# Kernel tuning notes

Measured on AMD Instinct MI355X. Metric: run time of the kernel, lower is better.

## Reference

```python
import jax, jax.numpy as jnp
import numpy as np

DIM = 1024
HEADS = 16
HEAD_DIM = DIM // HEADS
MLP_HID = 4 * DIM
EPS = 1e-5


def layer_norm(x, g, b):
    mu = jnp.mean(x, axis=-1, keepdims=True)
    var = jnp.mean(jnp.square(x - mu), axis=-1, keepdims=True)
    return (x - mu) * jax.lax.rsqrt(var + EPS) * g + b


def setup_inputs() -> dict:
    key = jax.random.key(0)
    ks = jax.random.split(key, 8)
    s_in = 1.0 / np.sqrt(DIM)
    s_hid = 1.0 / np.sqrt(MLP_HID)
    return {
        "x": jax.random.normal(ks[0], (4, 2048, DIM), dtype=jnp.float32),
        "qkv_w": jax.random.uniform(ks[1], (3 * DIM, DIM), jnp.float32, -s_in, s_in),
        "proj_w": jax.random.uniform(ks[2], (DIM, DIM), jnp.float32, -s_in, s_in),
        "proj_b": jnp.zeros((DIM,), jnp.float32),
        "ln1_g": jnp.ones((DIM,), jnp.float32),
        "ln1_b": jnp.zeros((DIM,), jnp.float32),
        "w1": jax.random.uniform(ks[3], (MLP_HID, DIM), jnp.float32, -s_in, s_in),
        "b1": jnp.zeros((MLP_HID,), jnp.float32),
        "prelu_a": jnp.asarray(0.25, jnp.float32),
        "w2": jax.random.uniform(ks[4], (DIM, MLP_HID), jnp.float32, -s_hid, s_hid),
        "b2": jnp.zeros((DIM,), jnp.float32),
        "ln2_g": jnp.ones((DIM,), jnp.float32),
        "ln2_b": jnp.zeros((DIM,), jnp.float32),
    }


def reference(x, qkv_w, proj_w, proj_b, ln1_g, ln1_b, w1, b1, prelu_a, w2, b2, ln2_g, ln2_b):
    B, N, C = x.shape
    scale = HEAD_DIM ** (-0.5)

    # Multi-head self-attention (full NxN scores, softmax over keys)
    qkv = (x @ qkv_w.T).reshape(B, N, 3, HEADS, HEAD_DIM)
    qkv = jnp.transpose(qkv, (2, 0, 3, 1, 4))  # [3, B, H, N, hd]
    q, k, v = qkv[0] * scale, qkv[1], qkv[2]
    attn = jax.nn.softmax(jnp.einsum("bhnd,bhmd->bhnm", q, k), axis=-1)
    o = jnp.einsum("bhnm,bhmd->bhnd", attn, v)
    o = jnp.transpose(o, (0, 2, 1, 3)).reshape(B, N, C)
    o = o @ proj_w.T + proj_b

    # Post-norm residual 1
    x = layer_norm(x + o, ln1_g, ln1_b)

    # MLP: Linear -> (Dropout=identity in eval) -> PReLU -> Linear
    h = x @ w1.T + b1
    h = jnp.where(h >= 0, h, prelu_a * h)
    h = h @ w2.T + b2

    # Post-norm residual 2
    return layer_norm(x + h, ln2_g, ln2_b)
```

## Files before the change

kernel.cpp:

```cpp
#include <hip/hip_runtime.h>


typedef __attribute__((ext_vector_type(8))) short short8;
typedef __attribute__((ext_vector_type(4))) short short4v;
typedef __attribute__((ext_vector_type(4))) float floatx4;
typedef __attribute__((ext_vector_type(4))) int int4v;

__device__ __forceinline__ float bf2f(unsigned short u) {
    return __uint_as_float(((unsigned int)u) << 16);
}
__device__ __forceinline__ unsigned short f2bf(float f) {
    unsigned int u = __float_as_uint(f);
    u += 0x7FFFu + ((u >> 16) & 1u);
    return (unsigned short)(u >> 16);
}
__device__ __forceinline__ int pack2bf(float a, float b) {
    return (int)f2bf(a) | ((int)f2bf(b) << 16);
}
__device__ __forceinline__ unsigned int cvt_pk_bf16(float lo, float hi) {
    unsigned int r;
    asm("v_cvt_pk_bf16_f32 %0, %1, %2" : "=v"(r) : "v"(lo), "v"(hi));
    return r;
}

#define Q_PRESCALE 0.18033688011112043f

#if __has_builtin(__builtin_amdgcn_exp2f)
__device__ __forceinline__ float fast_exp2(float x) { return __builtin_amdgcn_exp2f(x); }
#else
__device__ __forceinline__ float fast_exp2(float x) { return __expf(x * 0.6931471805599453f); }
#endif

#if __has_builtin(__builtin_amdgcn_permlane32_swap) && __has_builtin(__builtin_amdgcn_permlane16_swap)
#define HAVE_PERMLANE 1
#else
#define HAVE_PERMLANE 0
#endif

__device__ __forceinline__ void async16(const unsigned short* g, unsigned short* l) {
    __builtin_amdgcn_global_load_lds(
        (const __attribute__((address_space(1))) unsigned int*)g,
        (__attribute__((address_space(3))) unsigned int*)l, 16, 0, 0);
}

__global__ __launch_bounds__(256)
void cvt_f2b(const float* __restrict__ in, unsigned short* __restrict__ out) {
    const int i = (blockIdx.x * 256 + threadIdx.x) * 4;
    float4 v = *(const float4*)&in[i];
    short4v o;
    o[0] = (short)f2bf(v.x); o[1] = (short)f2bf(v.y);
    o[2] = (short)f2bf(v.z); o[3] = (short)f2bf(v.w);
    *(short4v*)&out[i] = o;
}

__global__ __launch_bounds__(512, 2)
void gemm256(const unsigned short* __restrict__ A,
             const unsigned short* __restrict__ W,
             const float* __restrict__ bias,
             const float* __restrict__ prelu,
             unsigned short* __restrict__ C,
             int N, int K, int qcols, int NNT) {
    __shared__ alignas(16) unsigned short lA[2][256 * 64];
    __shared__ alignas(16) unsigned short lB[2][256 * 64];

    const int nwg = gridDim.x;
    const int orig = blockIdx.x;
    const int q8 = nwg >> 3, r8 = nwg & 7, xx = orig & 7, rest = orig >> 3;
    const int wgid = (xx < r8 ? xx * (q8 + 1) : r8 * (q8 + 1) + (xx - r8) * q8) + rest;
    const int mt = wgid / NNT, nt = wgid % NNT;
    const int m0 = mt * 256, n0 = nt * 256;

    const int tid  = threadIdx.x;
    const int lane = tid & 63;
    const int wave = tid >> 6;
    const int lr = lane & 15, lq = lane >> 4;
    const int wrow = (wave >> 2) * 64;
    const int wcol = (wave & 3) * 32;
    const int srow = lane >> 3;
    const int scol = ((lane & 7) ^ srow) << 3;
    const int kx = lr & 7;

    const int NT = K >> 6;

    floatx4 acc[2][2][4][2] = {};

    auto stA = [&](int d, int tt, int h) {
        #pragma unroll
        for (int it = 0; it < 2; ++it) {
            const int rb = h * 128 + (wave * 2 + it) * 8;
            async16(&A[(size_t)(m0 + rb + srow) * K + tt * 64 + scol], &lA[d][rb * 64]);
        }
    };
    auto stB = [&](int d, int tt, int h) {
        #pragma unroll
        for (int it = 0; it < 2; ++it) {
            const int rb = h * 128 + (wave * 2 + it) * 8;
            async16(&W[(size_t)(n0 + rb + srow) * K + tt * 64 + scol], &lB[d][rb * 64]);
        }
    };

    stA(0, 0, 0); stB(0, 0, 0); stB(0, 0, 1); stA(0, 0, 1);
    stA(1, 1, 0); stB(1, 1, 0); stB(1, 1, 1);
    asm volatile("s_waitcnt vmcnt(6)" ::: "memory");
    __builtin_amdgcn_s_barrier();
    asm volatile("" ::: "memory");

    short8 af[4][2], b0[2][2], b1[2][2];

    for (int t = 0; t < NT; ++t) {
        const int d = t & 1, e = d ^ 1;

        #pragma unroll
        for (int i = 0; i < 4; ++i)
            #pragma unroll
            for (int s = 0; s < 2; ++s)
                af[i][s] = *(const short8*)&lA[d][(wrow + i * 16 + lr) * 64 +
                                                 (((s * 4 + lq) ^ kx) << 3)];
        #pragma unroll
        for (int j = 0; j < 2; ++j)
            #pragma unroll
            for (int s = 0; s < 2; ++s)
                b0[j][s] = *(const short8*)&lB[d][(wcol + j * 16 + lr) * 64 +
                                                 (((s * 4 + lq) ^ kx) << 3)];
        if (t + 1 < NT) stA(e, t + 1, 1);
        __builtin_amdgcn_s_barrier();
        asm volatile("s_waitcnt lgkmcnt(0)" ::: "memory");
        __builtin_amdgcn_s_setprio(1);
        #pragma unroll
        for (int s = 0; s < 2; ++s)
            #pragma unroll
            for (int i = 0; i < 4; ++i)
                #pragma unroll
                for (int j = 0; j < 2; ++j)
                    acc[0][0][i][j] = __builtin_amdgcn_mfma_f32_16x16x32_bf16(
                        af[i][s], b0[j][s], acc[0][0][i][j], 0, 0, 0);
        __builtin_amdgcn_s_setprio(0);
        __builtin_amdgcn_s_barrier();
        asm volatile("" ::: "memory");

        #pragma unroll
        for (int j = 0; j < 2; ++j)
            #pragma unroll
            for (int s = 0; s < 2; ++s)
                b1[j][s] = *(const short8*)&lB[d][(128 + wcol + j * 16 + lr) * 64 +
                                                 (((s * 4 + lq) ^ kx) << 3)];
        if (t + 2 < NT) stA(d, t + 2, 0);
        __builtin_amdgcn_s_barrier();
        asm volatile("s_waitcnt lgkmcnt(0)" ::: "memory");
        __builtin_amdgcn_s_setprio(1);
        #pragma unroll
        for (int s = 0; s < 2; ++s)
            #pragma unroll
            for (int i = 0; i < 4; ++i)
                #pragma unroll
                for (int j = 0; j < 2; ++j)
                    acc[0][1][i][j] = __builtin_amdgcn_mfma_f32_16x16x32_bf16(
                        af[i][s], b1[j][s], acc[0][1][i][j], 0, 0, 0);
        __builtin_amdgcn_s_setprio(0);
        __builtin_amdgcn_s_barrier();
        asm volatile("" ::: "memory");

        #pragma unroll
        for (int i = 0; i < 4; ++i)
            #pragma unroll
            for (int s = 0; s < 2; ++s)
                af[i][s] = *(const short8*)&lA[d][(128 + wrow + i * 16 + lr) * 64 +
                                                 (((s * 4 + lq) ^ kx) << 3)];
        if (t + 2 < NT) stB(d, t + 2, 0);
        __builtin_amdgcn_s_barrier();
        asm volatile("s_waitcnt lgkmcnt(0)" ::: "memory");
        __builtin_amdgcn_s_setprio(1);
        #pragma unroll
        for (int s = 0; s < 2; ++s)
            #pragma unroll
            for (int i = 0; i < 4; ++i)
                #pragma unroll
                for (int j = 0; j < 2; ++j)
                    acc[1][1][i][j] = __builtin_amdgcn_mfma_f32_16x16x32_bf16(
                        af[i][s], b1[j][s], acc[1][1][i][j], 0, 0, 0);
        __builtin_amdgcn_s_setprio(0);
        __builtin_amdgcn_s_barrier();
        asm volatile("" ::: "memory");

        if (t + 2 < NT) stB(d, t + 2, 1);
        __builtin_amdgcn_s_barrier();
        asm volatile("" ::: "memory");
        __builtin_amdgcn_s_setprio(1);
        #pragma unroll
        for (int s = 0; s < 2; ++s)
            #pragma unroll
            for (int i = 0; i < 4; ++i)
                #pragma unroll
                for (int j = 0; j < 2; ++j)
                    acc[1][0][i][j] = __builtin_amdgcn_mfma_f32_16x16x32_bf16(
                        af[i][s], b0[j][s], acc[1][0][i][j], 0, 0, 0);
        __builtin_amdgcn_s_setprio(0);
        if (t + 2 < NT) {
            asm volatile("s_waitcnt vmcnt(6)" ::: "memory");
        } else {
            asm volatile("s_waitcnt vmcnt(0)" ::: "memory");
        }
        __builtin_amdgcn_s_barrier();
        asm volatile("" ::: "memory");
    }

    const bool hasb = (bias != nullptr);
    const bool hasp = (prelu != nullptr);
    const float slope = hasp ? prelu[0] : 0.f;
    #pragma unroll
    for (int mh = 0; mh < 2; ++mh)
        #pragma unroll
        for (int nh = 0; nh < 2; ++nh)
            #pragma unroll
            for (int j = 0; j < 2; ++j) {
                const int gc = n0 + nh * 128 + wcol + j * 16 + lr;
                const float bv = hasb ? bias[gc] : 0.f;
                const float cs = (gc < qcols) ? Q_PRESCALE : 1.f;
                #pragma unroll
                for (int i = 0; i < 4; ++i) {
                    const int gr = m0 + mh * 128 + wrow + i * 16 + lq * 4;
                    #pragma unroll
                    for (int r = 0; r < 4; ++r) {
                        float v = acc[mh][nh][i][j][r] + bv;
                        if (hasp && v < 0.f) v *= slope;
                        C[(size_t)(gr + r) * N + gc] = f2bf(v * cs);
                    }
                }
            }
}

__global__ __launch_bounds__(512, 2)
void gemm128(const unsigned short* __restrict__ A,
             const unsigned short* __restrict__ W,
             const float* __restrict__ bias,
             const float* __restrict__ prelu,
             unsigned short* __restrict__ C,
             int N, int K, int qcols, int NNT) {
    __shared__ alignas(16) unsigned short lA[2][128 * 64];
    __shared__ alignas(16) unsigned short lB[2][256 * 64];

    const int nwg = gridDim.x;
    const int orig = blockIdx.x;
    const int q8 = nwg >> 3, r8 = nwg & 7, xx = orig & 7, rest = orig >> 3;
    const int wgid = (xx < r8 ? xx * (q8 + 1) : r8 * (q8 + 1) + (xx - r8) * q8) + rest;
    const int mt = wgid / NNT, nt = wgid % NNT;
    const int m0 = mt * 128, n0 = nt * 256;

    const int tid  = threadIdx.x;
    const int lane = tid & 63;
    const int wave = tid >> 6;
    const int lr = lane & 15, lq = lane >> 4;
    const int wrow = (wave >> 2) * 64;
    const int wcol = (wave & 3) * 32;
    const int srow = lane >> 3;
    const int scol = ((lane & 7) ^ srow) << 3;
    const int kx = lr & 7;

    const int NT = K >> 6;

    floatx4 acc[2][4][2] = {};

    auto stA = [&](int d, int tt) {
        #pragma unroll
        for (int it = 0; it < 2; ++it) {
            const int rb = (wave * 2 + it) * 8;
            async16(&A[(size_t)(m0 + rb + srow) * K + tt * 64 + scol], &lA[d][rb * 64]);
        }
    };
    auto stB = [&](int d, int tt, int h) {
        #pragma unroll
        for (int it = 0; it < 2; ++it) {
            const int rb = (wave * 2 + it) * 8;
            async16(&W[(size_t)(n0 + h * 128 + rb + srow) * K + tt * 64 + scol],
                    &lB[d][(h * 128 + rb) * 64]);
        }
    };

    stA(0, 0); stB(0, 0, 0); stB(0, 0, 1);
    stA(1, 1); stB(1, 1, 0);
    asm volatile("s_waitcnt vmcnt(4)" ::: "memory");
    __builtin_amdgcn_s_barrier();
    asm volatile("" ::: "memory");

    short8 af[4][2], b0[2][2], b1[2][2];

    for (int t = 0; t < NT; ++t) {
        const int d = t & 1, e = d ^ 1;

        #pragma unroll
        for (int i = 0; i < 4; ++i)
            #pragma unroll
            for (int s = 0; s < 2; ++s)
                af[i][s] = *(const short8*)&lA[d][(wrow + i * 16 + lr) * 64 +
                                                 (((s * 4 + lq) ^ kx) << 3)];
        #pragma unroll
        for (int j = 0; j < 2; ++j)
            #pragma unroll
            for (int s = 0; s < 2; ++s)
                b0[j][s] = *(const short8*)&lB[d][(wcol + j * 16 + lr) * 64 +
                                                 (((s * 4 + lq) ^ kx) << 3)];
        if (t + 1 < NT) stB(e, t + 1, 1);
        __builtin_amdgcn_s_barrier();
        asm volatile("s_waitcnt lgkmcnt(0)" ::: "memory");
        __builtin_amdgcn_s_setprio(1);
        #pragma unroll
        for (int s = 0; s < 2; ++s)
            #pragma unroll
            for (int i = 0; i < 4; ++i)
                #pragma unroll
                for (int j = 0; j < 2; ++j)
                    acc[0][i][j] = __builtin_amdgcn_mfma_f32_16x16x32_bf16(
                        af[i][s], b0[j][s], acc[0][i][j], 0, 0, 0);
        __builtin_amdgcn_s_setprio(0);
        __builtin_amdgcn_s_barrier();
        asm volatile("" ::: "memory");

        #pragma unroll
        for (int j = 0; j < 2; ++j)
            #pragma unroll
            for (int s = 0; s < 2; ++s)
                b1[j][s] = *(const short8*)&lB[d][(128 + wcol + j * 16 + lr) * 64 +
                                                 (((s * 4 + lq) ^ kx) << 3)];
        if (t + 2 < NT) { stA(d, t + 2); stB(d, t + 2, 0); }
        __builtin_amdgcn_s_barrier();
        asm volatile("s_waitcnt lgkmcnt(0)" ::: "memory");
        __builtin_amdgcn_s_setprio(1);
        #pragma unroll
        for (int s = 0; s < 2; ++s)
            #pragma unroll
            for (int i = 0; i < 4; ++i)
                #pragma unroll
                for (int j = 0; j < 2; ++j)
                    acc[1][i][j] = __builtin_amdgcn_mfma_f32_16x16x32_bf16(
                        af[i][s], b1[j][s], acc[1][i][j], 0, 0, 0);
        __builtin_amdgcn_s_setprio(0);
        if (t + 2 < NT) {
            asm volatile("s_waitcnt vmcnt(4)" ::: "memory");
        } else {
            asm volatile("s_waitcnt vmcnt(0)" ::: "memory");
        }
        __builtin_amdgcn_s_barrier();
        asm volatile("" ::: "memory");
    }

    const bool hasb = (bias != nullptr);
    const bool hasp = (prelu != nullptr);
    const float slope = hasp ? prelu[0] : 0.f;
    #pragma unroll
    for (int nh = 0; nh < 2; ++nh)
        #pragma unroll
        for (int j = 0; j < 2; ++j) {
            const int gc = n0 + nh * 128 + wcol + j * 16 + lr;
            const float bv = hasb ? bias[gc] : 0.f;
            const float cs = (gc < qcols) ? Q_PRESCALE : 1.f;
            #pragma unroll
            for (int i = 0; i < 4; ++i) {
                const int gr = m0 + wrow + i * 16 + lq * 4;
                #pragma unroll
                for (int r = 0; r < 4; ++r) {
                    float v = acc[nh][i][j][r] + bv;
                    if (hasp && v < 0.f) v *= slope;
                    C[(size_t)(gr + r) * N + gc] = f2bf(v * cs);
                }
            }
        }
}

__global__ __launch_bounds__(256)
void transpose_v(const unsigned short* __restrict__ qkv,
                 unsigned short* __restrict__ vt) {
    const int kt = blockIdx.x;
    const int bh = blockIdx.y;
    const int b = bh >> 4, h = bh & 15;
    __shared__ unsigned short tile[64 * 65];
    for (int t = threadIdx.x; t < 512; t += 256) {
        const int key = t >> 3, c8 = (t & 7) << 3;
        short8 v8 = *(const short8*)&qkv[((size_t)(b * 2048 + kt * 64 + key)) * 3072 +
                                         2048 + h * 64 + c8];
        #pragma unroll
        for (int e = 0; e < 8; ++e)
            tile[key * 65 + c8 + e] = (unsigned short)v8[e];
    }
    __syncthreads();
    for (int t = threadIdx.x; t < 512; t += 256) {
        const int d = t >> 3, k8 = (t & 7) << 3;
        short8 o;
        #pragma unroll
        for (int e = 0; e < 8; ++e)
            o[e] = (short)tile[(k8 + e) * 65 + d];
        *(short8*)&vt[((size_t)bh * 64 + d) * 2048 + kt * 64 + k8] = o;
    }
}

__global__ __launch_bounds__(256, 2)
void attn_kernel(const unsigned short* __restrict__ qkv,
                 const unsigned short* __restrict__ vt,
                 unsigned short* __restrict__ o_attn) {
    const int id = blockIdx.x;
    const int qg = id >> 6;
    const int bh = id & 63;
    const int b = bh >> 4, h = bh & 15;
    const int tid  = threadIdx.x;
    const int lane = tid & 63;
    const int wave = tid >> 6;
    const int lr = lane & 15;
    const int lq = lane >> 4;
    const int q0 = (qg * 4 + wave) * 64;
    const size_t row0 = (size_t)(b * 2048) * 3072;

    __shared__ alignas(16) unsigned short lK[2][64 * 64];
    __shared__ alignas(16) unsigned short lV[2][64 * 64];

    short8 qf[4][2];
    #pragma unroll
    for (int j = 0; j < 4; ++j)
        #pragma unroll
        for (int s = 0; s < 2; ++s)
            qf[j][s] = *(const short8*)&qkv[row0 + (size_t)(q0 + j * 16 + lr) * 3072 +
                                            h * 64 + s * 32 + lq * 8];

    floatx4 oacc[4][4] = {};
    float l_i[4] = {0.f, 0.f, 0.f, 0.f};

    const int srow = lane >> 3;
    const int scol = (((lane & 7) ^ srow)) << 3;
    const int kx = lr & 7;

    auto stage = [&](int bi, int kc) {
        #pragma unroll
        for (int it2 = 0; it2 < 2; ++it2) {
            const int it = wave * 2 + it2;
            const int row = it * 8 + srow;
            async16(&qkv[row0 + (size_t)(kc + row) * 3072 + 1024 + h * 64 + scol],
                    &lK[bi][it * 512 + lane * 8]);
            async16(&vt[((size_t)bh * 64 + row) * 2048 + kc + scol],
                    &lV[bi][it * 512 + lane * 8]);
        }
    };

    asm volatile("s_waitcnt vmcnt(0)" ::: "memory");
    stage(0, 0);

    #pragma unroll 1
    for (int c = 0; c < 32; ++c) {
        const int cur = c & 1;
        if (c + 1 < 32) {
            stage(cur ^ 1, (c + 1) * 64);
            asm volatile("s_waitcnt vmcnt(4)" ::: "memory");
        } else {
            asm volatile("s_waitcnt vmcnt(0)" ::: "memory");
        }
        __builtin_amdgcn_s_barrier();
        asm volatile("" ::: "memory");

        floatx4 sacc[4][4] = {};
        #pragma unroll
        for (int s = 0; s < 2; ++s) {
            short8 kf[4];
            #pragma unroll
            for (int i = 0; i < 4; ++i) {
                const int r = i * 16 + lr;
                kf[i] = *(const short8*)&lK[cur][r * 64 + (((s * 4 + lq) ^ kx) << 3)];
            }
            #pragma unroll
            for (int i = 0; i < 4; ++i)
                #pragma unroll
                for (int j = 0; j < 4; ++j)
                    sacc[i][j] = __builtin_amdgcn_mfma_f32_16x16x32_bf16(
                        kf[i], qf[j][s], sacc[i][j], 0, 0, 0);
        }

        unsigned int pkd[4][4][2];
        #pragma unroll
        for (int i = 0; i < 4; ++i)
            #pragma unroll
            for (int j = 0; j < 4; ++j) {
                const float e0 = fast_exp2(sacc[i][j][0]);
                const float e1 = fast_exp2(sacc[i][j][1]);
                const float e2 = fast_exp2(sacc[i][j][2]);
                const float e3 = fast_exp2(sacc[i][j][3]);
                l_i[j] += (e0 + e1) + (e2 + e3);
                pkd[i][j][0] = cvt_pk_bf16(e0, e1);
                pkd[i][j][1] = cvt_pk_bf16(e2, e3);
            }

        #pragma unroll
        for (int s = 0; s < 2; ++s) {
            short8 vf[4];
            #pragma unroll
            for (int i = 0; i < 4; ++i) {
                const int r = i * 16 + lr;
                vf[i] = *(const short8*)&lV[cur][r * 64 + (((s * 4 + lq) ^ kx) << 3)];
            }
            short8 bq[4];
            #pragma unroll
            for (int j = 0; j < 4; ++j) {
                int4v iv;
#if HAVE_PERMLANE
                auto p0 = __builtin_amdgcn_permlane32_swap(
                    pkd[2 * s][j][0], pkd[2 * s + 1][j][0], false, false);
                auto w0 = __builtin_amdgcn_permlane16_swap(p0[0], p0[1], false, false);
                auto p1 = __builtin_amdgcn_permlane32_swap(
                    pkd[2 * s][j][1], pkd[2 * s + 1][j][1], false, false);
                auto w1 = __builtin_amdgcn_permlane16_swap(p1[0], p1[1], false, false);
                iv[0] = (int)w0[0]; iv[1] = (int)w1[0];
                iv[2] = (int)w0[1]; iv[3] = (int)w1[1];
#else
                const int src0 = lr + ((lq & 1) * 2) * 16;
                const int src1 = src0 + 16;
                const bool hi = (lq >> 1) != 0;
                int a0 = __shfl((int)pkd[2 * s][j][0], src0, 64);
                int c0 = __shfl((int)pkd[2 * s + 1][j][0], src0, 64);
                int a1 = __shfl((int)pkd[2 * s][j][1], src0, 64);
                int c1 = __shfl((int)pkd[2 * s + 1][j][1], src0, 64);
                int a2 = __shfl((int)pkd[2 * s][j][0], src1, 64);
                int c2 = __shfl((int)pkd[2 * s + 1][j][0], src1, 64);
                int a3 = __shfl((int)pkd[2 * s][j][1], src1, 64);
                int c3 = __shfl((int)pkd[2 * s + 1][j][1], src1, 64);
                iv[0] = hi ? c0 : a0;
                iv[1] = hi ? c1 : a1;
                iv[2] = hi ? c2 : a2;
                iv[3] = hi ? c3 : a3;
#endif
                bq[j] = __builtin_bit_cast(short8, iv);
            }
            #pragma unroll
            for (int j = 0; j < 4; ++j)
                #pragma unroll
                for (int i = 0; i < 4; ++i)
                    oacc[i][j] = __builtin_amdgcn_mfma_f32_16x16x32_bf16(
                        vf[i], bq[j], oacc[i][j], 0, 0, 0);
        }

        asm volatile("s_waitcnt lgkmcnt(0)" ::: "memory");
        __builtin_amdgcn_s_barrier();
        asm volatile("" ::: "memory");
    }

    #pragma unroll
    for (int j = 0; j < 4; ++j) {
        l_i[j] += __shfl_xor(l_i[j], 16, 64);
        l_i[j] += __shfl_xor(l_i[j], 32, 64);
        const float rl = 1.f / l_i[j];
        const int q = q0 + j * 16 + lr;
        #pragma unroll
        for (int i = 0; i < 4; ++i) {
            int2 pk;
            pk.x = pack2bf(oacc[i][j][0] * rl, oacc[i][j][1] * rl);
            pk.y = pack2bf(oacc[i][j][2] * rl, oacc[i][j][3] * rl);
            *(int2*)&o_attn[((size_t)(b * 2048 + q)) * 1024 + h * 64 + i * 16 + lq * 4] = pk;
        }
    }
}

__global__ __launch_bounds__(256)
void ln_f32_bf16(const float* __restrict__ x,
                 const unsigned short* __restrict__ res,
                 const float* __restrict__ g,
                 const float* __restrict__ bta,
                 unsigned short* __restrict__ out) {
    const int row = blockIdx.x;
    const int t = threadIdx.x;
    const size_t base = (size_t)row * 1024;

    float4 xv = *(const float4*)&x[base + t * 4];
    short4v rv = *(const short4v*)&res[base + t * 4];
    float v[4] = { xv.x + bf2f((unsigned short)rv[0]),
                   xv.y + bf2f((unsigned short)rv[1]),
                   xv.z + bf2f((unsigned short)rv[2]),
                   xv.w + bf2f((unsigned short)rv[3]) };
    float s = 0.f, s2 = 0.f;
    #pragma unroll
    for (int k = 0; k < 4; ++k) { s += v[k]; s2 += v[k] * v[k]; }
    #pragma unroll
    for (int off = 32; off > 0; off >>= 1) {
        s  += __shfl_xor(s, off, 64);
        s2 += __shfl_xor(s2, off, 64);
    }
    __shared__ float red[8];
    const int wave = t >> 6;
    if ((t & 63) == 0) { red[wave] = s; red[4 + wave] = s2; }
    __syncthreads();
    s  = red[0] + red[1] + red[2] + red[3];
    s2 = red[4] + red[5] + red[6] + red[7];
    const float mean = s * (1.f / 1024.f);
    const float var  = fmaxf(s2 * (1.f / 1024.f) - mean * mean, 0.f);
    const float inv  = rsqrtf(var + 1e-5f);

    short4v ov;
    #pragma unroll
    for (int k = 0; k < 4; ++k) {
        int c = t * 4 + k;
        ov[k] = (short)f2bf((v[k] - mean) * inv * g[c] + bta[c]);
    }
    *(short4v*)&out[base + t * 4] = ov;
}

__global__ __launch_bounds__(256)
void ln_bf16_f32(const unsigned short* __restrict__ x,
                 const unsigned short* __restrict__ res,
                 const float* __restrict__ g,
                 const float* __restrict__ bta,
                 float* __restrict__ out) {
    const int row = blockIdx.x;
    const int t = threadIdx.x;
    const size_t base = (size_t)row * 1024;

    short4v xv = *(const short4v*)&x[base + t * 4];
    short4v rv = *(const short4v*)&res[base + t * 4];
    float v[4];
    float s = 0.f, s2 = 0.f;
    #pragma unroll
    for (int k = 0; k < 4; ++k) {
        v[k] = bf2f((unsigned short)xv[k]) + bf2f((unsigned short)rv[k]);
        s += v[k];
        s2 += v[k] * v[k];
    }
    #pragma unroll
    for (int off = 32; off > 0; off >>= 1) {
        s  += __shfl_xor(s, off, 64);
        s2 += __shfl_xor(s2, off, 64);
    }
    __shared__ float red[8];
    const int wave = t >> 6;
    if ((t & 63) == 0) { red[wave] = s; red[4 + wave] = s2; }
    __syncthreads();
    s  = red[0] + red[1] + red[2] + red[3];
    s2 = red[4] + red[5] + red[6] + red[7];
    const float mean = s * (1.f / 1024.f);
    const float var  = fmaxf(s2 * (1.f / 1024.f) - mean * mean, 0.f);
    const float inv  = rsqrtf(var + 1e-5f);

    float4 ov;
    ov.x = (v[0] - mean) * inv * g[t * 4 + 0] + bta[t * 4 + 0];
    ov.y = (v[1] - mean) * inv * g[t * 4 + 1] + bta[t * 4 + 1];
    ov.z = (v[2] - mean) * inv * g[t * 4 + 2] + bta[t * 4 + 2];
    ov.w = (v[3] - mean) * inv * g[t * 4 + 3] + bta[t * 4 + 3];
    *(float4*)&out[base + t * 4] = ov;
}

extern "C" void kernel_launch(void* const* d_in, const int* in_sizes, int n_in,
                              void* d_out, int out_size, void* d_ws, size_t ws_size,
                              hipStream_t stream) {
    const float* x      = (const float*)d_in[0];
    const float* qkv_w  = (const float*)d_in[1];
    const float* proj_w = (const float*)d_in[2];
    const float* proj_b = (const float*)d_in[3];
    const float* ln1_g  = (const float*)d_in[4];
    const float* ln1_b  = (const float*)d_in[5];
    const float* w1     = (const float*)d_in[6];
    const float* b1     = (const float*)d_in[7];
    const float* prelu  = (const float*)d_in[8];
    const float* w2     = (const float*)d_in[9];
    const float* b2     = (const float*)d_in[10];
    const float* ln2_g  = (const float*)d_in[11];
    const float* ln2_b  = (const float*)d_in[12];
    float* out = (float*)d_out;

    char* ws = (char*)d_ws;
    const size_t MB = 1024 * 1024;
    unsigned short* wqkvb  = (unsigned short*)(ws);
    unsigned short* wprojb = (unsigned short*)(ws + 6 * MB);
    unsigned short* w1b    = (unsigned short*)(ws + 8 * MB);
    unsigned short* w2b    = (unsigned short*)(ws + 16 * MB);
    unsigned short* xb     = (unsigned short*)(ws + 24 * MB);
    unsigned short* vtb    = (unsigned short*)(ws + 24 * MB);
    unsigned short* qkvb   = (unsigned short*)(ws + 40 * MB);
    unsigned short* oat    = (unsigned short*)(ws + 88 * MB);
    unsigned short* pout   = (unsigned short*)(ws + 24 * MB);
    unsigned short* x1b    = (unsigned short*)(ws + 40 * MB);
    unsigned short* h1     = (unsigned short*)(ws + 56 * MB);
    unsigned short* h2     = (unsigned short*)(ws + 24 * MB);

    cvt_f2b<<<8192, 256, 0, stream>>>(x,      xb);
    cvt_f2b<<<3072, 256, 0, stream>>>(qkv_w,  wqkvb);
    cvt_f2b<<<1024, 256, 0, stream>>>(proj_w, wprojb);
    cvt_f2b<<<4096, 256, 0, stream>>>(w1,     w1b);
    cvt_f2b<<<4096, 256, 0, stream>>>(w2,     w2b);

    gemm128<<<dim3(64 * 12), 512, 0, stream>>>(xb, wqkvb, nullptr, nullptr,
                                               qkvb, 3072, 1024, 1024, 12);
    transpose_v<<<dim3(32, 64), 256, 0, stream>>>(qkvb, vtb);
    attn_kernel<<<512, 256, 0, stream>>>(qkvb, vtb, oat);
    gemm128<<<dim3(64 * 4), 512, 0, stream>>>(oat, wprojb, proj_b, nullptr,
                                              pout, 1024, 1024, 0, 4);
    ln_f32_bf16<<<8192, 256, 0, stream>>>(x, pout, ln1_g, ln1_b, x1b);
    gemm256<<<dim3(32 * 16), 512, 0, stream>>>(x1b, w1b, b1, prelu,
                                               h1, 4096, 1024, 0, 16);
    gemm128<<<dim3(64 * 4), 512, 0, stream>>>(h1, w2b, b2, nullptr,
                                              h2, 1024, 4096, 0, 4);
    ln_bf16_f32<<<8192, 256, 0, stream>>>(x1b, h2, ln2_g, ln2_b, out);
}
```

Measured before the change: 485.8 us.

## Prefetch next-tile LDS fragments during MFMA phases in both GEMM kernels

Restructures the main loops of the 256- and 128-wide GEMM kernels so that LDS fragment reads for the next phase or next K-tile are issued before or after the preceding MFMA block rather than right before their own use. The explicit lgkmcnt(0) waits are removed, and the vmcnt waits move earlier so that the next tile's A/B fragments can be read at the end of the current iteration. The aim is to hide LDS read latency behind matrix-core work. The risk is subtle ordering hazards between the async global-to-LDS writes and the early reads, which now depend on compiler-inserted waits and the adjusted vmcnt counts.

```diff
diff --git a/kernel.cpp b/kernel.cpp
--- a/kernel.cpp
+++ b/kernel.cpp
@@ -42,6 +42,9 @@
         (const __attribute__((address_space(1))) unsigned int*)g,
         (__attribute__((address_space(3))) unsigned int*)l, 16, 0, 0);
 }
+
+#define BARRIER() do { __builtin_amdgcn_s_barrier(); asm volatile("" ::: "memory"); } while (0)
+#define VMCNT(n)  asm volatile("s_waitcnt vmcnt(" #n ")" ::: "memory")
 
 __global__ __launch_bounds__(256)
 void cvt_f2b(const float* __restrict__ in, unsigned short* __restrict__ out) {
@@ -83,6 +86,7 @@
     const int NT = K >> 6;
 
     floatx4 acc[2][2][4][2] = {};
+    short8 af[4][2], b0[2][2], b1[2][2];
 
     auto stA = [&](int d, int tt, int h) {
         #pragma unroll
@@ -99,110 +103,79 @@
         }
     };
 
+#define RD_AF(dd, half)                                                        \
+    _Pragma("unroll") for (int i = 0; i < 4; ++i)                              \
+    _Pragma("unroll") for (int s = 0; s < 2; ++s)                              \
+        af[i][s] = *(const short8*)&lA[dd][((half) * 128 + wrow + i * 16 + lr) * 64 + \
+                                           (((s * 4 + lq) ^ kx) << 3)]
+#define RD_B0(dd)                                                              \
+    _Pragma("unroll") for (int j = 0; j < 2; ++j)                              \
+    _Pragma("unroll") for (int s = 0; s < 2; ++s)                              \
+        b0[j][s] = *(const short8*)&lB[dd][(wcol + j * 16 + lr) * 64 +         \
+                                           (((s * 4 + lq) ^ kx) << 3)]
+#define RD_B1(dd)                                                              \
+    _Pragma("unroll") for (int j = 0; j < 2; ++j)                              \
+    _Pragma("unroll") for (int s = 0; s < 2; ++s)                              \
+        b1[j][s] = *(const short8*)&lB[dd][(128 + wcol + j * 16 + lr) * 64 +   \
+                                           (((s * 4 + lq) ^ kx) << 3)]
+#define MM256(mh, nh, BB)                                                      \
+    _Pragma("unroll") for (int s = 0; s < 2; ++s)                              \
+    _Pragma("unroll") for (int i = 0; i < 4; ++i)                              \
+    _Pragma("unroll") for (int j = 0; j < 2; ++j)                              \
+        acc[mh][nh][i][j] = __builtin_amdgcn_mfma_f32_16x16x32_bf16(           \
+            af[i][s], BB[j][s], acc[mh][nh][i][j], 0, 0, 0)
+
     stA(0, 0, 0); stB(0, 0, 0); stB(0, 0, 1); stA(0, 0, 1);
     stA(1, 1, 0); stB(1, 1, 0); stB(1, 1, 1);
-    asm volatile("s_waitcnt vmcnt(6)" ::: "memory");
-    __builtin_amdgcn_s_barrier();
-    asm volatile("" ::: "memory");
-
-    short8 af[4][2], b0[2][2], b1[2][2];
+    VMCNT(6);
+    BARRIER();
+    RD_AF(0, 0);
+    RD_B0(0);
 
     for (int t = 0; t < NT; ++t) {
         const int d = t & 1, e = d ^ 1;
 
-        #pragma unroll
-        for (int i = 0; i < 4; ++i)
-            #pragma unroll
-            for (int s = 0; s < 2; ++s)
-                af[i][s] = *(const short8*)&lA[d][(wrow + i * 16 + lr) * 64 +
-                                                 (((s * 4 + lq) ^ kx) << 3)];
-        #pragma unroll
-        for (int j = 0; j < 2; ++j)
-            #pragma unroll
-            for (int s = 0; s < 2; ++s)
-                b0[j][s] = *(const short8*)&lB[d][(wcol + j * 16 + lr) * 64 +
-                                                 (((s * 4 + lq) ^ kx) << 3)];
+        RD_B1(d);
         if (t + 1 < NT) stA(e, t + 1, 1);
-        __builtin_amdgcn_s_barrier();
-        asm volatile("s_waitcnt lgkmcnt(0)" ::: "memory");
+        BARRIER();
         __builtin_amdgcn_s_setprio(1);
-        #pragma unroll
-        for (int s = 0; s < 2; ++s)
-            #pragma unroll
-            for (int i = 0; i < 4; ++i)
-                #pragma unroll
-                for (int j = 0; j < 2; ++j)
-                    acc[0][0][i][j] = __builtin_amdgcn_mfma_f32_16x16x32_bf16(
-                        af[i][s], b0[j][s], acc[0][0][i][j], 0, 0, 0);
+        MM256(0, 0, b0);
         __builtin_amdgcn_s_setprio(0);
-        __builtin_amdgcn_s_barrier();
-        asm volatile("" ::: "memory");
-
-        #pragma unroll
-        for (int j = 0; j < 2; ++j)
-            #pragma unroll
-            for (int s = 0; s < 2; ++s)
-                b1[j][s] = *(const short8*)&lB[d][(128 + wcol + j * 16 + lr) * 64 +
-                                                 (((s * 4 + lq) ^ kx) << 3)];
+        BARRIER();
+
         if (t + 2 < NT) stA(d, t + 2, 0);
-        __builtin_amdgcn_s_barrier();
-        asm volatile("s_waitcnt lgkmcnt(0)" ::: "memory");
+        BARRIER();
         __builtin_amdgcn_s_setprio(1);
-        #pragma unroll
-        for (int s = 0; s < 2; ++s)
-            #pragma unroll
-            for (int i = 0; i < 4; ++i)
-                #pragma unroll
-                for (int j = 0; j < 2; ++j)
-                    acc[0][1][i][j] = __builtin_amdgcn_mfma_f32_16x16x32_bf16(
-                        af[i][s], b1[j][s], acc[0][1][i][j], 0, 0, 0);
+        MM256(0, 1, b1);
         __builtin_amdgcn_s_setprio(0);
-        __builtin_amdgcn_s_barrier();
-        asm volatile("" ::: "memory");
-
-        #pragma unroll
-        for (int i = 0; i < 4; ++i)
-            #pragma unroll
-            for (int s = 0; s < 2; ++s)
-                af[i][s] = *(const short8*)&lA[d][(128 + wrow + i * 16 + lr) * 64 +
-                                                 (((s * 4 + lq) ^ kx) << 3)];
+        RD_AF(d, 1);
+        BARRIER();
+
         if (t + 2 < NT) stB(d, t + 2, 0);
-        __builtin_amdgcn_s_barrier();
-        asm volatile("s_waitcnt lgkmcnt(0)" ::: "memory");
+        BARRIER();
         __builtin_amdgcn_s_setprio(1);
-        #pragma unroll
-        for (int s = 0; s < 2; ++s)
-            #pragma unroll
-            for (int i = 0; i < 4; ++i)
-                #pragma unroll
-                for (int j = 0; j < 2; ++j)
-                    acc[1][1][i][j] = __builtin_amdgcn_mfma_f32_16x16x32_bf16(
-                        af[i][s], b1[j][s], acc[1][1][i][j], 0, 0, 0);
+        MM256(1, 1, b1);
         __builtin_amdgcn_s_setprio(0);
-        __builtin_amdgcn_s_barrier();
-        asm volatile("" ::: "memory");
+        if (t + 2 < NT)      { VMCNT(4); }
+        else if (t + 1 < NT) { VMCNT(0); }
+        BARRIER();
 
         if (t + 2 < NT) stB(d, t + 2, 1);
-        __builtin_amdgcn_s_barrier();
-        asm volatile("" ::: "memory");
+        BARRIER();
         __builtin_amdgcn_s_setprio(1);
-        #pragma unroll
-        for (int s = 0; s < 2; ++s)
-            #pragma unroll
-            for (int i = 0; i < 4; ++i)
-                #pragma unroll
-                for (int j = 0; j < 2; ++j)
-                    acc[1][0][i][j] = __builtin_amdgcn_mfma_f32_16x16x32_bf16(
-                        af[i][s], b0[j][s], acc[1][0][i][j], 0, 0, 0);
+        MM256(1, 0, b0);
         __builtin_amdgcn_s_setprio(0);
-        if (t + 2 < NT) {
-            asm volatile("s_waitcnt vmcnt(6)" ::: "memory");
-        } else {
-            asm volatile("s_waitcnt vmcnt(0)" ::: "memory");
-        }
-        __builtin_amdgcn_s_barrier();
-        asm volatile("" ::: "memory");
-    }
+        if (t + 1 < NT) {
+            RD_AF(e, 0);
+            RD_B0(e);
+        }
+        BARRIER();
+    }
+
+#undef RD_AF
+#undef RD_B0
+#undef RD_B1
+#undef MM256
 
     const bool hasb = (bias != nullptr);
     const bool hasp = (prelu != nullptr);
@@ -259,6 +232,7 @@
     const int NT = K >> 6;
 
     floatx4 acc[2][4][2] = {};
+    short8 af[4][2], b0[2][2], b1[2][2];
 
     auto stA = [&](int d, int tt) {
         #pragma unroll
@@ -276,72 +250,65 @@
         }
     };
 
+#define RD_AF(dd)                                                              \
+    _Pragma("unroll") for (int i = 0; i < 4; ++i)                              \
+    _Pragma("unroll") for (int s = 0; s < 2; ++s)                              \
+        af[i][s] = *(const short8*)&lA[dd][(wrow + i * 16 + lr) * 64 +         \
+                                           (((s * 4 + lq) ^ kx) << 3)]
+#define RD_B0(dd)                                                              \
+    _Pragma("unroll") for (int j = 0; j < 2; ++j)                              \
+    _Pragma("unroll") for (int s = 0; s < 2; ++s)                              \
+        b0[j][s] = *(const short8*)&lB[dd][(wcol + j * 16 + lr) * 64 +         \
+                                           (((s * 4 + lq) ^ kx) << 3)]
+#define RD_B1(dd)                                                              \
+    _Pragma("unroll") for (int j = 0; j < 2; ++j)                              \
+    _Pragma("unroll") for (int s = 0; s < 2; ++s)                              \
+        b1[j][s] = *(const short8*)&lB[dd][(128 + wcol + j * 16 + lr) * 64 +   \
+                                           (((s * 4 + lq) ^ kx) << 3)]
+#define MM128(nh, BB)                                                          \
+    _Pragma("unroll") for (int s = 0; s < 2; ++s)                              \
+    _Pragma("unroll") for (int i = 0; i < 4; ++i)                              \
+    _Pragma("unroll") for (int j = 0; j < 2; ++j)                              \
+        acc[nh][i][j] = __builtin_amdgcn_mfma_f32_16x16x32_bf16(               \
+            af[i][s], BB[j][s], acc[nh][i][j], 0, 0, 0)
+
     stA(0, 0); stB(0, 0, 0); stB(0, 0, 1);
     stA(1, 1); stB(1, 1, 0);
-    asm volatile("s_waitcnt vmcnt(4)" ::: "memory");
-    __builtin_amdgcn_s_barrier();
-    asm volatile("" ::: "memory");
-
-    short8 af[4][2], b0[2][2], b1[2][2];
+    VMCNT(4);
+    BARRIER();
+    RD_AF(0);
+    RD_B0(0);
 
     for (int t = 0; t < NT; ++t) {
         const int d = t & 1, e = d ^ 1;
 
-        #pragma unroll
-        for (int i = 0; i < 4; ++i)
-            #pragma unroll
-            for (int s = 0; s < 2; ++s)
-                af[i][s] = *(const short8*)&lA[d][(wrow + i * 16 + lr) * 64 +
-                                                 (((s * 4 + lq) ^ kx) << 3)];
-        #pragma unroll
-        for (int j = 0; j < 2; ++j)
-            #pragma unroll
-            for (int s = 0; s < 2; ++s)
-                b0[j][s] = *(const short8*)&lB[d][(wcol + j * 16 + lr) * 64 +
-                                                 (((s * 4 + lq) ^ kx) << 3)];
+        RD_B1(d);
         if (t + 1 < NT) stB(e, t + 1, 1);
-        __builtin_amdgcn_s_barrier();
-        asm volatile("s_waitcnt lgkmcnt(0)" ::: "memory");
+        BARRIER();
         __builtin_amdgcn_s_setprio(1);
-        #pragma unroll
-        for (int s = 0; s < 2; ++s)
-            #pragma unroll
-            for (int i = 0; i < 4; ++i)
-                #pragma unroll
-                for (int j = 0; j < 2; ++j)
-                    acc[0][i][j] = __builtin_amdgcn_mfma_f32_16x16x32_bf16(
-                        af[i][s], b0[j][s], acc[0][i][j], 0, 0, 0);
+        MM128(0, b0);
         __builtin_amdgcn_s_setprio(0);
-        __builtin_amdgcn_s_barrier();
-        asm volatile("" ::: "memory");
-
-        #pragma unroll
-        for (int j = 0; j < 2; ++j)
-            #pragma unroll
-            for (int s = 0; s < 2; ++s)
-                b1[j][s] = *(const short8*)&lB[d][(128 + wcol + j * 16 + lr) * 64 +
-                                                 (((s * 4 + lq) ^ kx) << 3)];
+        if (t + 1 < NT) { VMCNT(2); }
+        BARRIER();
+
         if (t + 2 < NT) { stA(d, t + 2); stB(d, t + 2, 0); }
-        __builtin_amdgcn_s_barrier();
-        asm volatile("s_waitcnt lgkmcnt(0)" ::: "memory");
+        BARRIER();
         __builtin_amdgcn_s_setprio(1);
-        #pragma unroll
-        for (int s = 0; s < 2; ++s)
-            #pragma unroll
-            for (int i = 0; i < 4; ++i)
-                #pragma unroll
-                for (int j = 0; j < 2; ++j)
-                    acc[1][i][j] = __builtin_amdgcn_mfma_f32_16x16x32_bf16(
-                        af[i][s], b1[j][s], acc[1][i][j], 0, 0, 0);
+        MM128(1, b1);
         __builtin_amdgcn_s_setprio(0);
-        if (t + 2 < NT) {
-            asm volatile("s_waitcnt vmcnt(4)" ::: "memory");
-        } else {
-            asm volatile("s_waitcnt vmcnt(0)" ::: "memory");
-        }
-        __builtin_amdgcn_s_barrier();
-        asm volatile("" ::: "memory");
-    }
+        if (t + 2 < NT)      { VMCNT(4); }
+        else if (t + 1 < NT) { VMCNT(0); }
+        if (t + 1 < NT) {
+            RD_AF(e);
+            RD_B0(e);
+        }
+        BARRIER();
+    }
+
+#undef RD_AF
+#undef RD_B0
+#undef RD_B1
+#undef MM128
 
     const bool hasb = (bias != nullptr);
     const bool hasp = (prelu != nullptr);
```

Measured after the change: 506.0 us. 4.2% more time.
